# Kernel optimization log

Measured on AMD Instinct MI355X. Metric: run time of the kernel, lower is better.

The kernel has to match this reference:

```python
import jax, jax.numpy as jnp
import numpy as np

B, L, D, H = 4, 2048, 1024, 16
HD = D // H


def setup_inputs() -> dict:
    key = jax.random.key(0)
    k1, k2, k3 = jax.random.split(key, 3)
    x = jax.random.normal(k1, (B, L, D), dtype=jnp.float32)
    # causal mask: True means masked (matches masked_fill semantics)
    attn_mask = jnp.triu(jnp.ones((L, L), dtype=bool), k=1)
    # xavier-ish init scale
    w_qkv = jax.random.normal(k2, (D, 3 * D), dtype=jnp.float32) * 0.02
    w_proj = jax.random.normal(k3, (D, D), dtype=jnp.float32) * 0.02
    b_proj = jnp.zeros((D,), dtype=jnp.float32)
    return {"x": x, "attn_mask": attn_mask, "w_qkv": w_qkv, "w_proj": w_proj, "b_proj": b_proj}


def reference(x, attn_mask, w_qkv, w_proj, b_proj):
    b, l, d = x.shape
    h, hd = H, HD
    scale = hd ** -0.5
    qkv = x @ w_qkv                                  # (B, L, 3D)
    qkv = qkv.reshape(b, l, 3, h, hd)
    q = qkv[:, :, 0].transpose(0, 2, 1, 3)           # (B, H, L, hd)
    k = qkv[:, :, 1].transpose(0, 2, 1, 3)
    v = qkv[:, :, 2].transpose(0, 2, 1, 3)
    attn = jnp.einsum('bhqd,bhkd->bhqk', q, k) * scale
    attn = jnp.where(attn_mask[None, None, :, :], -jnp.inf, attn)
    attn = jax.nn.softmax(attn, axis=-1)             # dropout is identity at eval
    out = jnp.einsum('bhqk,bhkd->bhqd', attn, v)     # (B, H, L, hd)
    out = out.transpose(0, 2, 1, 3).reshape(b, l, d)
    return out @ w_proj + b_proj
```

## Files before the change

kernel.cpp:

```cpp
#include <hip/hip_runtime.h>
#include <stdint.h>

#define B_ 4
#define L_ 2048
#define D_ 1024
#define H_ 16
#define HD_ 64
#define M_ (B_*L_)
#define N3_ (3*D_)

typedef _Float16 h8 __attribute__((ext_vector_type(8)));
typedef _Float16 h4v __attribute__((ext_vector_type(4)));
typedef float f4 __attribute__((ext_vector_type(4)));
typedef float f16v __attribute__((ext_vector_type(16)));
typedef unsigned int u32x4 __attribute__((ext_vector_type(4)));

__device__ __forceinline__ void gload16(const void* g, void* l) {
  __builtin_amdgcn_global_load_lds(
      (const __attribute__((address_space(1))) void*)g,
      (__attribute__((address_space(3))) void*)l, 16, 0, 0);
}

__global__ void k_cvt_f16(const float* __restrict__ in, _Float16* __restrict__ out, int n4) {
  int i = blockIdx.x*blockDim.x + threadIdx.x;
  int st = gridDim.x*blockDim.x;
  for (; i < n4; i += st) {
    float4 v = ((const float4*)in)[i];
    h4v o = { (_Float16)v.x, (_Float16)v.y, (_Float16)v.z, (_Float16)v.w };
    ((h4v*)out)[i] = o;
  }
}

__global__ void k_transpose_f16(const float* __restrict__ in, _Float16* __restrict__ out, int R, int C) {
  __shared__ float tile[32][33];
  int bc = blockIdx.x*32, br = blockIdx.y*32;
  int tx = threadIdx.x, ty = threadIdx.y;
  #pragma unroll
  for (int j = 0; j < 32; j += 8)
    tile[ty+j][tx] = in[(size_t)(br+ty+j)*C + bc+tx];
  __syncthreads();
  #pragma unroll
  for (int j = 0; j < 32; j += 8)
    out[(size_t)(bc+ty+j)*R + br+tx] = (_Float16)tile[tx][ty+j];
}

__global__ __launch_bounds__(256,2)
void k_vtrans(const _Float16* __restrict__ Vi, _Float16* __restrict__ Vo) {
  __shared__ _Float16 T[64*64];
  int bh = blockIdx.x >> 5, lt = blockIdx.x & 31;
  int tid = threadIdx.x;
  const _Float16* src = Vi + ((size_t)bh*L_ + lt*64)*64;
  #pragma unroll
  for (int i = 0; i < 2; ++i) {
    int s = tid + i*256;
    int row = s >> 3;
    int swz = (row & 7) ^ ((row >> 3) & 7);
    int c8 = ((s & 7) ^ swz) * 8;
    gload16(src + row*64 + c8, (char*)T + s*16);
  }
  __syncthreads();
  #pragma unroll
  for (int i = 0; i < 2; ++i) {
    int s = tid + i*256;
    int d = s >> 3, c = s & 7;
    h8 v;
    #pragma unroll
    for (int k = 0; k < 8; ++k) {
      int l = c*8 + k;
      int swz = (l & 7) ^ ((l >> 3) & 7);
      int byteoff = (l*8 + ((d >> 3) ^ swz))*16 + (d & 7)*2;
      v[k] = *(const _Float16*)((const char*)T + byteoff);
    }
    *(h8*)(Vo + ((size_t)bh*64 + d)*L_ + lt*64 + c*8) = v;
  }
}

template<int EPI>
__global__ __launch_bounds__(256,2)
void k_gemm(const _Float16* __restrict__ A, const _Float16* __restrict__ Bt,
            float* __restrict__ Cf, const float* __restrict__ bias,
            _Float16* __restrict__ Qo, _Float16* __restrict__ Ko, _Float16* __restrict__ Vo,
            int N, int K, int nbn) {
  __shared__ _Float16 Al[128*64];
  __shared__ _Float16 Bl[128*64];
  int cpx = gridDim.x >> 3;
  int bid = (blockIdx.x & 7)*cpx + (blockIdx.x >> 3);
  int bm = bid / nbn, bn = bid % nbn;
  int tid = threadIdx.x;
  int lane = tid & 63;
  int wm = tid >> 7, wn = (tid >> 6) & 1;
  int g = lane >> 4, cl = lane & 15;
  f4 acc[4][4] = {};
  const _Float16* Ab = A + (size_t)bm*128*K;
  const _Float16* Bb = Bt + (size_t)bn*128*K;
  int s_row[4], s_off[4];
  #pragma unroll
  for (int i = 0; i < 4; ++i) {
    int s = tid + i*256;
    s_row[i] = s >> 3;
    s_off[i] = ((s & 7) ^ (s_row[i] & 7)) * 8;
  }
  for (int kt = 0; kt < K; kt += 64) {
    #pragma unroll
    for (int i = 0; i < 4; ++i) {
      int s = tid + i*256;
      gload16(Ab + (size_t)s_row[i]*K + kt + s_off[i], (char*)Al + s*16);
      gload16(Bb + (size_t)s_row[i]*K + kt + s_off[i], (char*)Bl + s*16);
    }
    __syncthreads();
    #pragma unroll
    for (int kk = 0; kk < 2; ++kk) {
      h8 af[4], bf[4];
      #pragma unroll
      for (int mi = 0; mi < 4; ++mi) {
        int row = wm*64 + mi*16 + cl;
        int c = (kk*4 + g) ^ (row & 7);
        af[mi] = *(const h8*)((const char*)Al + row*128 + c*16);
      }
      #pragma unroll
      for (int ni = 0; ni < 4; ++ni) {
        int row = wn*64 + ni*16 + cl;
        int c = (kk*4 + g) ^ (row & 7);
        bf[ni] = *(const h8*)((const char*)Bl + row*128 + c*16);
      }
      #pragma unroll
      for (int mi = 0; mi < 4; ++mi)
        #pragma unroll
        for (int ni = 0; ni < 4; ++ni)
          acc[mi][ni] = __builtin_amdgcn_mfma_f32_16x16x32_f16(af[mi], bf[ni], acc[mi][ni], 0, 0, 0);
    }
    __syncthreads();
  }
  if (EPI == 1) {
    float bsv[4];
    #pragma unroll
    for (int ni = 0; ni < 4; ++ni) bsv[ni] = bias[bn*128 + wn*64 + ni*16 + cl];
    #pragma unroll
    for (int mi = 0; mi < 4; ++mi)
      #pragma unroll
      for (int r = 0; r < 4; ++r) {
        int m = bm*128 + wm*64 + mi*16 + g*4 + r;
        float* orow = Cf + (size_t)m*N + bn*128 + wn*64 + cl;
        #pragma unroll
        for (int ni = 0; ni < 4; ++ni)
          orow[ni*16] = acc[mi][ni][r] + bsv[ni];
      }
  } else {
    int region = (bn*128) >> 10;
    _Float16* P = (region == 0) ? Qo : (region == 1) ? Ko : Vo;
    float scl = (region == 0) ? 0.18033688011112042f : 1.0f;
    #pragma unroll
    for (int mi = 0; mi < 4; ++mi)
      #pragma unroll
      for (int r = 0; r < 4; ++r) {
        int m = bm*128 + wm*64 + mi*16 + g*4 + r;
        int b = m >> 11, l = m & 2047;
        #pragma unroll
        for (int ni = 0; ni < 4; ++ni) {
          int n = bn*128 + wn*64 + ni*16 + cl;
          int cc = n & 1023;
          int h = cc >> 6, d = cc & 63;
          P[(((size_t)b*16 + h)*2048 + l)*64 + d] = (_Float16)(acc[mi][ni][r] * scl);
        }
      }
  }
}

__global__ __launch_bounds__(256,2)
void k_attn(const _Float16* __restrict__ Q, const _Float16* __restrict__ K,
            const _Float16* __restrict__ Vt, _Float16* __restrict__ Oo) {
  __shared__ _Float16 Kl[2][64*64];
  __shared__ _Float16 Vl[2][64*64];
  int bid = blockIdx.x;
  int bh = bid & 63;
  int qt = 15 - (bid >> 6);
  int tid = threadIdx.x, lane = tid & 63, w = tid >> 6;
  int l31 = lane & 31, hf = lane >> 5;
  int qbase = qt*128;
  int qw = qbase + w*32;
  int q = qw + l31;
  const _Float16* Qh = Q + (size_t)bh*L_*HD_;
  const _Float16* Kh = K + (size_t)bh*L_*HD_;
  const _Float16* Vh = Vt + (size_t)bh*HD_*L_;
  int srow[2], sc8[2];
  #pragma unroll
  for (int i = 0; i < 2; ++i) {
    int s = tid + i*256;
    srow[i] = s >> 3;
    sc8[i] = ((s & 7) ^ (srow[i] & 7)) * 8;
  }
  h8 qf[4];
  #pragma unroll
  for (int kd = 0; kd < 4; ++kd)
    qf[kd] = *(const h8*)(Qh + (size_t)q*64 + kd*16 + hf*8);
  f16v oacc[2] = {};
  float mrun = -1e30f, lrun = 0.f;
  int ntiles = (qbase >> 6) + 2;

  auto stage = [&](int t, int buf) {
    int kv0s = t*64;
    #pragma unroll
    for (int i = 0; i < 2; ++i) {
      int s = tid + i*256;
      gload16(Kh + (size_t)(kv0s + srow[i])*64 + sc8[i], (char*)&Kl[buf][0] + s*16);
      gload16(Vh + (size_t)srow[i]*L_ + kv0s + sc8[i], (char*)&Vl[buf][0] + s*16);
    }
  };
  stage(0, 0);
  for (int t = 0; t < ntiles; ++t) {
    __syncthreads();
    if (t + 1 < ntiles) stage(t + 1, (t + 1) & 1);
    int kv0 = t*64;
    if (kv0 <= qw + 31) {
      const char* Kb = (const char*)&Kl[t & 1][0];
      const char* Vb = (const char*)&Vl[t & 1][0];
      f16v st[2] = {};
      __builtin_amdgcn_s_setprio(1);
      #pragma unroll
      for (int kb = 0; kb < 2; ++kb)
        #pragma unroll
        for (int kd = 0; kd < 4; ++kd) {
          int r = kb*32 + l31;
          int c = (kd*2 + hf) ^ (r & 7);
          h8 kf = *(const h8*)(Kb + r*128 + c*16);
          st[kb] = __builtin_amdgcn_mfma_f32_32x32x16_f16(kf, qf[kd], st[kb], 0, 0, 0);
        }
      __builtin_amdgcn_s_setprio(0);
      bool needm = (kv0 + 63) > qw;
      float p[2][16];
      #pragma unroll
      for (int kb = 0; kb < 2; ++kb)
        #pragma unroll
        for (int rg = 0; rg < 16; ++rg) {
          float v = st[kb][rg];
          if (needm) {
            int kv = kv0 + kb*32 + (rg & 3) + 8*(rg >> 2) + 4*hf;
            if (kv > q) v = -1e30f;
          }
          p[kb][rg] = v;
        }
      float rm = -1e30f;
      #pragma unroll
      for (int kb = 0; kb < 2; ++kb)
        #pragma unroll
        for (int rg = 0; rg < 16; ++rg) rm = fmaxf(rm, p[kb][rg]);
      rm = fmaxf(rm, __shfl_xor(rm, 32));
      if (!__all(rm <= mrun + 8.f)) {
        float mnew = fmaxf(mrun, rm);
        float corr = exp2f(mrun - mnew);
        mrun = mnew;
        lrun *= corr;
        #pragma unroll
        for (int db = 0; db < 2; ++db)
          #pragma unroll
          for (int rg = 0; rg < 16; ++rg) oacc[db][rg] *= corr;
      }
      float rs = 0.f;
      #pragma unroll
      for (int kb = 0; kb < 2; ++kb)
        #pragma unroll
        for (int rg = 0; rg < 16; ++rg) {
          float e = exp2f(p[kb][rg] - mrun);
          p[kb][rg] = e;
          rs += e;
        }
      rs += __shfl_xor(rs, 32);
      lrun += rs;
      h8 pb[4];
      #pragma unroll
      for (int blk = 0; blk < 4; ++blk) {
        int kb = blk >> 1, sb = (blk & 1)*8;
        unsigned dw0 = __builtin_bit_cast(unsigned, __builtin_amdgcn_cvt_pkrtz(p[kb][sb+0], p[kb][sb+1]));
        unsigned dw1 = __builtin_bit_cast(unsigned, __builtin_amdgcn_cvt_pkrtz(p[kb][sb+2], p[kb][sb+3]));
        unsigned dw2 = __builtin_bit_cast(unsigned, __builtin_amdgcn_cvt_pkrtz(p[kb][sb+4], p[kb][sb+5]));
        unsigned dw3 = __builtin_bit_cast(unsigned, __builtin_amdgcn_cvt_pkrtz(p[kb][sb+6], p[kb][sb+7]));
        unsigned eu = hf ? dw0 : dw2;
        unsigned ev = hf ? dw1 : dw3;
        unsigned up = (unsigned)__shfl_xor((int)eu, 32);
        unsigned vp = (unsigned)__shfl_xor((int)ev, 32);
        u32x4 tmp;
        if (hf == 0) tmp = (u32x4){dw0, dw1, up, vp};
        else         tmp = (u32x4){up, vp, dw2, dw3};
        pb[blk] = __builtin_bit_cast(h8, tmp);
      }
      __builtin_amdgcn_s_setprio(1);
      #pragma unroll
      for (int db = 0; db < 2; ++db)
        #pragma unroll
        for (int ks = 0; ks < 4; ++ks) {
          int r = db*32 + l31;
          int c = (ks*2 + hf) ^ (r & 7);
          h8 vf = *(const h8*)(Vb + r*128 + c*16);
          oacc[db] = __builtin_amdgcn_mfma_f32_32x32x16_f16(vf, pb[ks], oacc[db], 0, 0, 0);
        }
      __builtin_amdgcn_s_setprio(0);
    }
  }
  float inv = 1.0f / lrun;
  int b = bh >> 4, hh = bh & 15;
  _Float16* obase = Oo + (((size_t)b*L_ + q)*H_ + hh)*HD_;
  #pragma unroll
  for (int db = 0; db < 2; ++db)
    #pragma unroll
    for (int grp = 0; grp < 4; ++grp) {
      unsigned lo = __builtin_bit_cast(unsigned,
          __builtin_amdgcn_cvt_pkrtz(oacc[db][grp*4+0]*inv, oacc[db][grp*4+1]*inv));
      unsigned hi = __builtin_bit_cast(unsigned,
          __builtin_amdgcn_cvt_pkrtz(oacc[db][grp*4+2]*inv, oacc[db][grp*4+3]*inv));
      uint2 qq; qq.x = lo; qq.y = hi;
      *(uint2*)(obase + db*32 + grp*8 + 4*hf) = qq;
    }
}

extern "C" void kernel_launch(void* const* d_in, const int* in_sizes, int n_in,
                              void* d_out, int out_size, void* d_ws, size_t ws_size,
                              hipStream_t stream) {
  const float* x      = (const float*)d_in[0];
  const float* w_qkv  = (const float*)d_in[2];
  const float* w_proj = (const float*)d_in[3];
  const float* b_proj = (const float*)d_in[4];
  float* out = (float*)d_out;
  char* ws = (char*)d_ws;
  _Float16* xh     = (_Float16*)(ws);
  _Float16* wqkvT  = (_Float16*)(ws + 16777216);
  _Float16* wprojT = (_Float16*)(ws + 23068672);
  _Float16* Qb     = (_Float16*)(ws + 25165824);
  _Float16* Kb     = (_Float16*)(ws + 41943040);
  _Float16* Vtmp   = (_Float16*)(ws + 58720256);
  _Float16* Vtb    = xh;
  _Float16* AOb    = Vtmp;

  k_cvt_f16<<<2048, 256, 0, stream>>>(x, xh, (B_*L_*D_)/4);
  k_transpose_f16<<<dim3(N3_/32, D_/32), dim3(32,8), 0, stream>>>(w_qkv, wqkvT, D_, N3_);
  k_transpose_f16<<<dim3(D_/32, D_/32), dim3(32,8), 0, stream>>>(w_proj, wprojT, D_, D_);
  k_gemm<0><<<(M_/128)*(N3_/128), 256, 0, stream>>>(xh, wqkvT, nullptr, nullptr,
                                                    Qb, Kb, Vtmp, N3_, D_, N3_/128);
  k_vtrans<<<2048, 256, 0, stream>>>(Vtmp, Vtb);
  k_attn<<<1024, 256, 0, stream>>>(Qb, Kb, Vtb, AOb);
  k_gemm<1><<<(M_/128)*(D_/128), 256, 0, stream>>>(AOb, wprojT, out, b_proj,
                                                   nullptr, nullptr, nullptr, D_, D_, D_/128);
}
```

Measured before the change: 274.4 us.

## Replace QKV GEMM with 256x256 tile, 8-wave, double-buffered pipelined kernel

Splits the templated GEMM into a dedicated QKV projection kernel and a projection kernel. The QKV kernel uses 256x256 output tiles with 512 threads and double-buffered LDS staging in quarter chunks, interleaving global-to-LDS loads with MFMA phases using explicit vmcnt waits and barriers. This is meant to hide global load latency and raise data reuse per tile. In exchange it uses more LDS (128KB) and many more accumulator registers, which may limit occupancy. The other edits are small cleanups through a pack helper.

```diff
diff --git a/kernel.cpp b/kernel.cpp
--- a/kernel.cpp
+++ b/kernel.cpp
@@ -15,10 +15,18 @@
 typedef float f16v __attribute__((ext_vector_type(16)));
 typedef unsigned int u32x4 __attribute__((ext_vector_type(4)));
 
+#define BAR() asm volatile("s_barrier" ::: "memory")
+#define WAIT_VM2() asm volatile("s_waitcnt vmcnt(2)" ::: "memory")
+#define WAIT_VM0() asm volatile("s_waitcnt vmcnt(0)" ::: "memory")
+
 __device__ __forceinline__ void gload16(const void* g, void* l) {
   __builtin_amdgcn_global_load_lds(
       (const __attribute__((address_space(1))) void*)g,
       (__attribute__((address_space(3))) void*)l, 16, 0, 0);
+}
+
+__device__ __forceinline__ unsigned pkh(float a, float b) {
+  return __builtin_bit_cast(unsigned, __builtin_amdgcn_cvt_pkrtz(a, b));
 }
 
 __global__ void k_cvt_f16(const float* __restrict__ in, _Float16* __restrict__ out, int n4) {
@@ -75,12 +83,110 @@
   }
 }
 
-template<int EPI>
+__global__ __launch_bounds__(512,2)
+void k_gemm_qkv(const _Float16* __restrict__ A, const _Float16* __restrict__ Bt,
+                _Float16* __restrict__ Qo, _Float16* __restrict__ Ko, _Float16* __restrict__ Vo) {
+  __shared__ __align__(16) _Float16 SA[2*2*128*64];
+  __shared__ __align__(16) _Float16 SB[2*2*128*64];
+  const int NBN = 12, NT = 16;
+  int cpx = gridDim.x >> 3;
+  int bid = (blockIdx.x & 7)*cpx + (blockIdx.x >> 3);
+  int bm = bid / NBN, bn = bid % NBN;
+  int tid = threadIdx.x;
+  int lane = tid & 63;
+  int wv = tid >> 6, wm = wv >> 2, wn = wv & 3;
+  int g = lane >> 4, cl = lane & 15;
+  const _Float16* Ab = A + (size_t)bm*256*1024;
+  const _Float16* Bb = Bt + (size_t)bn*256*1024;
+  int r0 = tid >> 3,         c0 = ((tid & 7) ^ (r0 & 7)) * 8;
+  int r1 = (tid + 512) >> 3, c1 = (((tid + 512) & 7) ^ (r1 & 7)) * 8;
+  int dst0 = tid*16, dst1 = (tid + 512)*16;
+  f4 acc[8][4] = {};
+  h8 af[4][2], bfr[4][2];
+
+  auto stage = [&](int j, int tw) {
+    int half = j & 1;
+    const _Float16* gb = (j >> 1) ? Bb : Ab;
+    char* lb = (char*)((j >> 1) ? SB : SA) + ((tw & 1)*2 + half)*16384;
+    gload16(gb + (size_t)(half*128 + r0)*1024 + tw*64 + c0, lb + dst0);
+    gload16(gb + (size_t)(half*128 + r1)*1024 + tw*64 + c1, lb + dst1);
+  };
+  auto readA = [&](int buf, int qm) {
+    const char* base = (const char*)SA + (buf*2 + wm)*16384;
+    #pragma unroll
+    for (int mi = 0; mi < 4; ++mi) {
+      int row = qm*64 + mi*16 + cl;
+      #pragma unroll
+      for (int kk = 0; kk < 2; ++kk) {
+        int c = (kk*4 + g) ^ (row & 7);
+        af[mi][kk] = *(const h8*)(base + row*128 + c*16);
+      }
+    }
+  };
+  auto readB = [&](int buf, int qn) {
+    const char* base = (const char*)SB + (buf*2 + (wn >> 1))*16384;
+    #pragma unroll
+    for (int ni = 0; ni < 2; ++ni) {
+      int row = (wn & 1)*64 + (qn*2 + ni)*16 + cl;
+      #pragma unroll
+      for (int kk = 0; kk < 2; ++kk) {
+        int c = (kk*4 + g) ^ (row & 7);
+        bfr[qn*2 + ni][kk] = *(const h8*)(base + row*128 + c*16);
+      }
+    }
+  };
+  auto mm = [&](int qm, int qn) {
+    __builtin_amdgcn_s_setprio(1);
+    #pragma unroll
+    for (int kk = 0; kk < 2; ++kk)
+      #pragma unroll
+      for (int mi = 0; mi < 4; ++mi)
+        #pragma unroll
+        for (int ni = 0; ni < 2; ++ni)
+          acc[qm*4 + mi][qn*2 + ni] = __builtin_amdgcn_mfma_f32_16x16x32_f16(
+              af[mi][kk], bfr[qn*2 + ni][kk], acc[qm*4 + mi][qn*2 + ni], 0, 0, 0);
+    __builtin_amdgcn_s_setprio(0);
+  };
+
+  stage(0,0); stage(1,0); stage(2,0); stage(3,0);
+  stage(0,1);
+  WAIT_VM2(); BAR();
+  for (int T = 0; T < NT; ++T) {
+    int buf = T & 1;
+    bool more1 = (T + 1 < NT);
+    readA(buf, 0); readB(buf, 0);
+    if (more1) stage(1, T + 1);
+    BAR(); mm(0, 0); BAR();
+    readB(buf, 1);
+    if (more1) stage(2, T + 1);
+    BAR(); mm(0, 1); BAR();
+    readA(buf, 1);
+    if (more1) stage(3, T + 1);
+    BAR(); mm(1, 0); BAR();
+    if (T + 2 < NT) { stage(0, T + 2); WAIT_VM2(); } else { WAIT_VM0(); }
+    BAR(); mm(1, 1); BAR();
+  }
+  int region = bn >> 2;
+  _Float16* P = (region == 0) ? Qo : (region == 1) ? Ko : Vo;
+  float scl = (region == 0) ? 0.18033688011112042f : 1.0f;
+  #pragma unroll
+  for (int mi = 0; mi < 8; ++mi)
+    #pragma unroll
+    for (int r = 0; r < 4; ++r) {
+      int m = bm*256 + wm*128 + mi*16 + g*4 + r;
+      int b = m >> 11, l = m & 2047;
+      #pragma unroll
+      for (int ni = 0; ni < 4; ++ni) {
+        int col = bn*256 + wn*64 + ni*16 + cl;
+        int h = (col >> 6) & 15, d = col & 63;
+        P[(((size_t)b*16 + h)*2048 + l)*64 + d] = (_Float16)(acc[mi][ni][r] * scl);
+      }
+    }
+}
+
 __global__ __launch_bounds__(256,2)
-void k_gemm(const _Float16* __restrict__ A, const _Float16* __restrict__ Bt,
-            float* __restrict__ Cf, const float* __restrict__ bias,
-            _Float16* __restrict__ Qo, _Float16* __restrict__ Ko, _Float16* __restrict__ Vo,
-            int N, int K, int nbn) {
+void k_gemm_proj(const _Float16* __restrict__ A, const _Float16* __restrict__ Bt,
+                 float* __restrict__ Cf, const float* __restrict__ bias, int N, int K, int nbn) {
   __shared__ _Float16 Al[128*64];
   __shared__ _Float16 Bl[128*64];
   int cpx = gridDim.x >> 3;
@@ -110,60 +216,40 @@
     __syncthreads();
     #pragma unroll
     for (int kk = 0; kk < 2; ++kk) {
-      h8 af[4], bf[4];
+      h8 a2[4], b2[4];
       #pragma unroll
       for (int mi = 0; mi < 4; ++mi) {
         int row = wm*64 + mi*16 + cl;
         int c = (kk*4 + g) ^ (row & 7);
-        af[mi] = *(const h8*)((const char*)Al + row*128 + c*16);
+        a2[mi] = *(const h8*)((const char*)Al + row*128 + c*16);
       }
       #pragma unroll
       for (int ni = 0; ni < 4; ++ni) {
         int row = wn*64 + ni*16 + cl;
         int c = (kk*4 + g) ^ (row & 7);
-        bf[ni] = *(const h8*)((const char*)Bl + row*128 + c*16);
+        b2[ni] = *(const h8*)((const char*)Bl + row*128 + c*16);
       }
       #pragma unroll
       for (int mi = 0; mi < 4; ++mi)
         #pragma unroll
         for (int ni = 0; ni < 4; ++ni)
-          acc[mi][ni] = __builtin_amdgcn_mfma_f32_16x16x32_f16(af[mi], bf[ni], acc[mi][ni], 0, 0, 0);
+          acc[mi][ni] = __builtin_amdgcn_mfma_f32_16x16x32_f16(a2[mi], b2[ni], acc[mi][ni], 0, 0, 0);
     }
     __syncthreads();
   }
-  if (EPI == 1) {
-    float bsv[4];
-    #pragma unroll
-    for (int ni = 0; ni < 4; ++ni) bsv[ni] = bias[bn*128 + wn*64 + ni*16 + cl];
-    #pragma unroll
-    for (int mi = 0; mi < 4; ++mi)
-      #pragma unroll
-      for (int r = 0; r < 4; ++r) {
-        int m = bm*128 + wm*64 + mi*16 + g*4 + r;
-        float* orow = Cf + (size_t)m*N + bn*128 + wn*64 + cl;
-        #pragma unroll
-        for (int ni = 0; ni < 4; ++ni)
-          orow[ni*16] = acc[mi][ni][r] + bsv[ni];
-      }
-  } else {
-    int region = (bn*128) >> 10;
-    _Float16* P = (region == 0) ? Qo : (region == 1) ? Ko : Vo;
-    float scl = (region == 0) ? 0.18033688011112042f : 1.0f;
-    #pragma unroll
-    for (int mi = 0; mi < 4; ++mi)
-      #pragma unroll
-      for (int r = 0; r < 4; ++r) {
-        int m = bm*128 + wm*64 + mi*16 + g*4 + r;
-        int b = m >> 11, l = m & 2047;
-        #pragma unroll
-        for (int ni = 0; ni < 4; ++ni) {
-          int n = bn*128 + wn*64 + ni*16 + cl;
-          int cc = n & 1023;
-          int h = cc >> 6, d = cc & 63;
-          P[(((size_t)b*16 + h)*2048 + l)*64 + d] = (_Float16)(acc[mi][ni][r] * scl);
-        }
-      }
-  }
+  float bsv[4];
+  #pragma unroll
+  for (int ni = 0; ni < 4; ++ni) bsv[ni] = bias[bn*128 + wn*64 + ni*16 + cl];
+  #pragma unroll
+  for (int mi = 0; mi < 4; ++mi)
+    #pragma unroll
+    for (int r = 0; r < 4; ++r) {
+      int m = bm*128 + wm*64 + mi*16 + g*4 + r;
+      float* orow = Cf + (size_t)m*N + bn*128 + wn*64 + cl;
+      #pragma unroll
+      for (int ni = 0; ni < 4; ++ni)
+        orow[ni*16] = acc[mi][ni][r] + bsv[ni];
+    }
 }
 
 __global__ __launch_bounds__(256,2)
@@ -270,10 +356,10 @@
       #pragma unroll
       for (int blk = 0; blk < 4; ++blk) {
         int kb = blk >> 1, sb = (blk & 1)*8;
-        unsigned dw0 = __builtin_bit_cast(unsigned, __builtin_amdgcn_cvt_pkrtz(p[kb][sb+0], p[kb][sb+1]));
-        unsigned dw1 = __builtin_bit_cast(unsigned, __builtin_amdgcn_cvt_pkrtz(p[kb][sb+2], p[kb][sb+3]));
-        unsigned dw2 = __builtin_bit_cast(unsigned, __builtin_amdgcn_cvt_pkrtz(p[kb][sb+4], p[kb][sb+5]));
-        unsigned dw3 = __builtin_bit_cast(unsigned, __builtin_amdgcn_cvt_pkrtz(p[kb][sb+6], p[kb][sb+7]));
+        unsigned dw0 = pkh(p[kb][sb+0], p[kb][sb+1]);
+        unsigned dw1 = pkh(p[kb][sb+2], p[kb][sb+3]);
+        unsigned dw2 = pkh(p[kb][sb+4], p[kb][sb+5]);
+        unsigned dw3 = pkh(p[kb][sb+6], p[kb][sb+7]);
         unsigned eu = hf ? dw0 : dw2;
         unsigned ev = hf ? dw1 : dw3;
         unsigned up = (unsigned)__shfl_xor((int)eu, 32);
@@ -303,11 +389,9 @@
   for (int db = 0; db < 2; ++db)
     #pragma unroll
     for (int grp = 0; grp < 4; ++grp) {
-      unsigned lo = __builtin_bit_cast(unsigned,
-          __builtin_amdgcn_cvt_pkrtz(oacc[db][grp*4+0]*inv, oacc[db][grp*4+1]*inv));
-      unsigned hi = __builtin_bit_cast(unsigned,
-          __builtin_amdgcn_cvt_pkrtz(oacc[db][grp*4+2]*inv, oacc[db][grp*4+3]*inv));
-      uint2 qq; qq.x = lo; qq.y = hi;
+      uint2 qq;
+      qq.x = pkh(oacc[db][grp*4+0]*inv, oacc[db][grp*4+1]*inv);
+      qq.y = pkh(oacc[db][grp*4+2]*inv, oacc[db][grp*4+3]*inv);
       *(uint2*)(obase + db*32 + grp*8 + 4*hf) = qq;
     }
 }
@@ -333,10 +417,8 @@
   k_cvt_f16<<<2048, 256, 0, stream>>>(x, xh, (B_*L_*D_)/4);
   k_transpose_f16<<<dim3(N3_/32, D_/32), dim3(32,8), 0, stream>>>(w_qkv, wqkvT, D_, N3_);
   k_transpose_f16<<<dim3(D_/32, D_/32), dim3(32,8), 0, stream>>>(w_proj, wprojT, D_, D_);
-  k_gemm<0><<<(M_/128)*(N3_/128), 256, 0, stream>>>(xh, wqkvT, nullptr, nullptr,
-                                                    Qb, Kb, Vtmp, N3_, D_, N3_/128);
+  k_gemm_qkv<<<(M_/256)*(N3_/256), 512, 0, stream>>>(xh, wqkvT, Qb, Kb, Vtmp);
   k_vtrans<<<2048, 256, 0, stream>>>(Vtmp, Vtb);
   k_attn<<<1024, 256, 0, stream>>>(Qb, Kb, Vtb, AOb);
-  k_gemm<1><<<(M_/128)*(D_/128), 256, 0, stream>>>(AOb, wprojT, out, b_proj,
-                                                   nullptr, nullptr, nullptr, D_, D_, D_/128);
-}
+  k_gemm_proj<<<(M_/128)*(D_/128), 256, 0, stream>>>(AOb, wprojT, out, b_proj, D_, D_, D_/128);
+}
```

After: 276.2 us. Within noise of the previous version (+0.6%).
